# Optimization experiments

Hardware: AMD Instinct MI355X
Metric: run time of the kernel (lower is better)

## Reference

```python
import jax, jax.numpy as jnp
import numpy as np

DK = 64

def setup_inputs() -> dict:
    key = jax.random.key(0)
    kx, kq, kk, kv = jax.random.split(key, 4)
    B, T, DM, DV = 256, 256, 384, 64
    x = jax.random.normal(kx, (B, T, DM), dtype=jnp.float32)
    s = 1.0 / np.sqrt(DM)
    W_q = jax.random.normal(kq, (DM, DK), dtype=jnp.float32) * s
    W_k = jax.random.normal(kk, (DM, DK), dtype=jnp.float32) * s
    W_v = jax.random.normal(kv, (DM, DV), dtype=jnp.float32) * s
    return {"x": x, "W_q": W_q, "W_k": W_k, "W_v": W_v}

def reference(x, W_q, W_k, W_v):
    # x: [B, T, dm]; projections to [B, T, dk]/[B, T, dv]
    q = jnp.einsum('btc,ck->btk', x, W_q)
    k = jnp.einsum('btc,ck->btk', x, W_k)
    v = jnp.einsum('btc,cv->btv', x, W_v)
    scale = k.shape[-1] ** (-0.5)
    wei = jnp.einsum('btk,bsk->bts', q, k) * scale  # [B, T, T]
    T = x.shape[1]
    causal = jnp.tril(jnp.ones((T, T), dtype=bool))
    wei = jnp.where(causal, wei, -jnp.inf)
    wei = jax.nn.softmax(wei, axis=-1)
    # dropout omitted (eval mode / deterministic reference)
    out = jnp.einsum('bts,bsv->btv', wei, v)
    return out
```

## Files before the change

### kernel.cpp

```cpp
#include <hip/hip_runtime.h>


typedef __attribute__((ext_vector_type(8))) short short8;
typedef __attribute__((ext_vector_type(4))) float floatx4;

__device__ inline unsigned short f2bf(float f) {
  union { float f; unsigned u; } v; v.f = f;
  unsigned r = v.u + 0x7FFFu + ((v.u >> 16) & 1u);
  return (unsigned short)(r >> 16);
}

__global__ void wt_kernel(const float* __restrict__ wq, const float* __restrict__ wk,
                          const float* __restrict__ wv, unsigned short* __restrict__ wt) {
  int idx = blockIdx.x * 256 + threadIdx.x;
  if (idx >= 3 * 384 * 64) return;
  int mat = idx / (384 * 64);
  int rem = idx % (384 * 64);
  int k = rem >> 6, n = rem & 63;
  const float* w = (mat == 0) ? wq : ((mat == 1) ? wk : wv);
  wt[((size_t)mat * 64 + n) * 384 + k] = f2bf(w[rem]);
}

__global__ __launch_bounds__(256) void qkv_kernel(
    const float* __restrict__ x, const unsigned short* __restrict__ wt,
    unsigned short* __restrict__ q, unsigned short* __restrict__ k2,
    unsigned short* __restrict__ v) {
  int lane = threadIdx.x & 63;
  int wave = threadIdx.x >> 6;
  int m = lane & 15, quad = lane >> 4;
  int tokBase = blockIdx.x * 128 + wave * 32;

  floatx4 z = {0.f, 0.f, 0.f, 0.f};
  floatx4 acc[2][12];
#pragma unroll
  for (int a = 0; a < 2; ++a)
#pragma unroll
    for (int b = 0; b < 12; ++b) acc[a][b] = z;

#pragma unroll
  for (int ks = 0; ks < 12; ++ks) {
    short8 af[2];
#pragma unroll
    for (int mt = 0; mt < 2; ++mt) {
      const float* ap = x + (size_t)(tokBase + mt * 16 + m) * 384 + ks * 32 + quad * 8;
      float4 x0 = *(const float4*)ap;
      float4 x1 = *(const float4*)(ap + 4);
      short8 t;
      t[0] = (short)f2bf(x0.x); t[1] = (short)f2bf(x0.y);
      t[2] = (short)f2bf(x0.z); t[3] = (short)f2bf(x0.w);
      t[4] = (short)f2bf(x1.x); t[5] = (short)f2bf(x1.y);
      t[6] = (short)f2bf(x1.z); t[7] = (short)f2bf(x1.w);
      af[mt] = t;
    }
#pragma unroll
    for (int nt = 0; nt < 12; ++nt) {
      const short8 bf = *(const short8*)&wt[((size_t)(nt >> 2) * 64 + (nt & 3) * 16 + m) * 384 + ks * 32 + quad * 8];
      acc[0][nt] = __builtin_amdgcn_mfma_f32_16x16x32_bf16(af[0], bf, acc[0][nt], 0, 0, 0);
      acc[1][nt] = __builtin_amdgcn_mfma_f32_16x16x32_bf16(af[1], bf, acc[1][nt], 0, 0, 0);
    }
  }

#pragma unroll
  for (int mt = 0; mt < 2; ++mt)
#pragma unroll
    for (int nt = 0; nt < 12; ++nt) {
      unsigned short* op = (nt < 4) ? q : ((nt < 8) ? k2 : v);
      int ncol = (nt & 3) * 16;
#pragma unroll
      for (int j = 0; j < 4; ++j) {
        int row = tokBase + mt * 16 + quad * 4 + j;
        op[(size_t)row * 64 + ncol + m] = f2bf(acc[mt][nt][j]);
      }
    }
}

__global__ __launch_bounds__(256) void attn_kernel(
    const unsigned short* __restrict__ Q, const unsigned short* __restrict__ K,
    const unsigned short* __restrict__ V, float* __restrict__ out) {
  __shared__ __align__(16) unsigned short sK[256 * 72];
  __shared__ __align__(16) unsigned short sV[64 * 264];

  int tid = threadIdx.x;
  int lane = tid & 63, wave = tid >> 6;
  int m = lane & 15, quad = lane >> 4;
  int b = blockIdx.x >> 2, qt = blockIdx.x & 3;

  const unsigned short* Kg = K + (size_t)b * 256 * 64;
#pragma unroll
  for (int it = 0; it < 8; ++it) {
    int s = it * 32 + (tid >> 3);
    int c = (tid & 7) * 8;
    *(uint4*)&sK[s * 72 + c] = *(const uint4*)&Kg[s * 64 + c];
  }
  const unsigned short* Vg = V + (size_t)b * 256 * 64;
#pragma unroll 4
  for (int it = 0; it < 64; ++it) {
    int idx = it * 256 + tid;
    sV[(idx & 63) * 264 + (idx >> 6)] = Vg[idx];
  }

  int qrow = qt * 64 + wave * 16 + m;
  const unsigned short* Qg = Q + ((size_t)b * 256 + qrow) * 64;
  short8 qf0 = *(const short8*)&Qg[quad * 8];
  short8 qf1 = *(const short8*)&Qg[32 + quad * 8];

  __syncthreads();

  floatx4 z = {0.f, 0.f, 0.f, 0.f};
  floatx4 sacc[16];
#pragma unroll
  for (int nt = 0; nt < 16; ++nt) sacc[nt] = z;
#pragma unroll
  for (int nt = 0; nt < 16; ++nt) {
    short8 kb0 = *(const short8*)&sK[(nt * 16 + m) * 72 + quad * 8];
    short8 kb1 = *(const short8*)&sK[(nt * 16 + m) * 72 + 32 + quad * 8];
    sacc[nt] = __builtin_amdgcn_mfma_f32_16x16x32_bf16(qf0, kb0, sacc[nt], 0, 0, 0);
    sacc[nt] = __builtin_amdgcn_mfma_f32_16x16x32_bf16(qf1, kb1, sacc[nt], 0, 0, 0);
  }

  const float CSC = 0.18033688011112042f;
  const float NEG = -3.0e38f;
  float inv[4];
  int rbase = qt * 64 + wave * 16 + quad * 4;
#pragma unroll
  for (int j = 0; j < 4; ++j) {
    int rg = rbase + j;
    float mx = NEG;
#pragma unroll
    for (int nt = 0; nt < 16; ++nt) {
      int col = nt * 16 + m;
      float sv = sacc[nt][j];
      if (col > rg) { sv = NEG; sacc[nt][j] = sv; }
      mx = fmaxf(mx, sv);
    }
    mx = fmaxf(mx, __shfl_xor(mx, 1));
    mx = fmaxf(mx, __shfl_xor(mx, 2));
    mx = fmaxf(mx, __shfl_xor(mx, 4));
    mx = fmaxf(mx, __shfl_xor(mx, 8));
    float sum = 0.f;
#pragma unroll
    for (int nt = 0; nt < 16; ++nt) {
      float p = exp2f((sacc[nt][j] - mx) * CSC);
      sacc[nt][j] = p;
      sum += p;
    }
    sum += __shfl_xor(sum, 1);
    sum += __shfl_xor(sum, 2);
    sum += __shfl_xor(sum, 4);
    sum += __shfl_xor(sum, 8);
    inv[j] = 1.f / sum;
  }

  __syncthreads();

  unsigned short* sP = sK + wave * (16 * 264);
#pragma unroll
  for (int nt = 0; nt < 16; ++nt)
#pragma unroll
    for (int j = 0; j < 4; ++j)
      sP[(quad * 4 + j) * 264 + nt * 16 + m] = f2bf(sacc[nt][j] * inv[j]);

  __syncthreads();

  floatx4 o[4];
#pragma unroll
  for (int vt = 0; vt < 4; ++vt) o[vt] = z;
#pragma unroll
  for (int ks = 0; ks < 8; ++ks) {
    short8 pf = *(const short8*)&sP[m * 264 + ks * 32 + quad * 8];
#pragma unroll
    for (int vt = 0; vt < 4; ++vt) {
      short8 vb = *(const short8*)&sV[(vt * 16 + m) * 264 + ks * 32 + quad * 8];
      o[vt] = __builtin_amdgcn_mfma_f32_16x16x32_bf16(pf, vb, o[vt], 0, 0, 0);
    }
  }

  float* op = out + ((size_t)b * 256 + qt * 64 + wave * 16) * 64;
#pragma unroll
  for (int vt = 0; vt < 4; ++vt)
#pragma unroll
    for (int j = 0; j < 4; ++j)
      op[(quad * 4 + j) * 64 + vt * 16 + m] = o[vt][j];
}

extern "C" void kernel_launch(void* const* d_in, const int* in_sizes, int n_in,
                              void* d_out, int out_size, void* d_ws, size_t ws_size,
                              hipStream_t stream) {
  const float* x  = (const float*)d_in[0];
  const float* wq = (const float*)d_in[1];
  const float* wk = (const float*)d_in[2];
  const float* wv = (const float*)d_in[3];
  float* out = (float*)d_out;

  unsigned short* wt = (unsigned short*)d_ws;
  unsigned short* q  = (unsigned short*)((char*)d_ws + 147456);
  unsigned short* k  = q + (size_t)65536 * 64;
  unsigned short* v  = k + (size_t)65536 * 64;

  wt_kernel<<<288, 256, 0, stream>>>(wq, wk, wv, wt);
  qkv_kernel<<<512, 256, 0, stream>>>(x, wt, q, k, v);
  attn_kernel<<<256 * 4, 256, 0, stream>>>(q, k, v, out);
}
```

Measured before the change: 209.9 us.

## Stage QKV projection tiles via async LDS loads and emit transposed V

The QKV projection kernel now double-buffers x and weight tiles in LDS using global_load_lds with XOR swizzles. Each block handles 64 tokens, and each wave owns 48 output columns instead of reading operands straight from global memory per wave. V is written transposed through an LDS tile, so the attention kernel can load it with 16-byte vector copies instead of scalar transposing stores. The weight-transpose kernel is also remapped so its writes are coalesced. Together these aim to cut redundant global traffic and the slow scalar V transpose, at the cost of more LDS use and extra barriers.

Measured after the change: 194.5 us. 7.3% less time.

```diff
diff --git a/kernel.cpp b/kernel.cpp
--- a/kernel.cpp
+++ b/kernel.cpp
@@ -10,73 +10,129 @@
   return (unsigned short)(r >> 16);
 }
 
+__device__ inline void glds16(const void* g, void* l) {
+  __builtin_amdgcn_global_load_lds(
+      (const __attribute__((address_space(1))) void*)g,
+      (__attribute__((address_space(3))) void*)l, 16, 0, 0);
+}
+
 __global__ void wt_kernel(const float* __restrict__ wq, const float* __restrict__ wk,
                           const float* __restrict__ wv, unsigned short* __restrict__ wt) {
   int idx = blockIdx.x * 256 + threadIdx.x;
-  if (idx >= 3 * 384 * 64) return;
-  int mat = idx / (384 * 64);
-  int rem = idx % (384 * 64);
-  int k = rem >> 6, n = rem & 63;
+  if (idx >= 3 * 64 * 384) return;
+  int mat = idx / (64 * 384);
+  int rem = idx % (64 * 384);
+  int n = rem / 384, k = rem % 384;
   const float* w = (mat == 0) ? wq : ((mat == 1) ? wk : wv);
-  wt[((size_t)mat * 64 + n) * 384 + k] = f2bf(w[rem]);
-}
-
-__global__ __launch_bounds__(256) void qkv_kernel(
+  wt[idx] = f2bf(w[k * 64 + n]);
+}
+
+__global__ __launch_bounds__(256, 4) void qkv_kernel(
     const float* __restrict__ x, const unsigned short* __restrict__ wt,
-    unsigned short* __restrict__ q, unsigned short* __restrict__ k2,
-    unsigned short* __restrict__ v) {
-  int lane = threadIdx.x & 63;
-  int wave = threadIdx.x >> 6;
+    unsigned short* __restrict__ q, unsigned short* __restrict__ kk,
+    unsigned short* __restrict__ vt) {
+  __shared__ __align__(16) float          xa[2][64 * 32];
+  __shared__ __align__(16) unsigned short wb[2][192 * 32];
+
+  int tid = threadIdx.x, lane = tid & 63, w = tid >> 6;
   int m = lane & 15, quad = lane >> 4;
-  int tokBase = blockIdx.x * 128 + wave * 32;
+  int tok0 = blockIdx.x * 64;
 
   floatx4 z = {0.f, 0.f, 0.f, 0.f};
-  floatx4 acc[2][12];
-#pragma unroll
-  for (int a = 0; a < 2; ++a)
-#pragma unroll
-    for (int b = 0; b < 12; ++b) acc[a][b] = z;
-
-#pragma unroll
+  floatx4 acc[4][3];
+#pragma unroll
+  for (int a = 0; a < 4; ++a)
+#pragma unroll
+    for (int b = 0; b < 3; ++b) acc[a][b] = z;
+
+  auto stage = [&](int ks, int buf) {
+#pragma unroll
+    for (int i = 0; i < 2; ++i) {
+      int a = w * 2 + i;
+      int row = a * 8 + (lane >> 3);
+      int kq = (lane & 7) ^ (row & 7);
+      glds16(x + (size_t)(tok0 + row) * 384 + ks * 32 + kq * 4,
+             (void*)&xa[buf][a * 256]);
+    }
+#pragma unroll
+    for (int i = 0; i < 3; ++i) {
+      int g = w * 3 + i;
+      int c = g * 16 + (lane >> 2);
+      int kq = (lane & 3) ^ (c & 3) ^ ((c >> 2) & 3);
+      glds16(wt + (size_t)c * 384 + ks * 32 + kq * 8,
+             (void*)&wb[buf][g * 512]);
+    }
+  };
+
+  stage(0, 0);
+#pragma unroll 1
   for (int ks = 0; ks < 12; ++ks) {
-    short8 af[2];
-#pragma unroll
-    for (int mt = 0; mt < 2; ++mt) {
-      const float* ap = x + (size_t)(tokBase + mt * 16 + m) * 384 + ks * 32 + quad * 8;
-      float4 x0 = *(const float4*)ap;
-      float4 x1 = *(const float4*)(ap + 4);
+    int buf = ks & 1;
+    __syncthreads();
+    if (ks < 11) stage(ks + 1, buf ^ 1);
+
+    short8 af[4];
+#pragma unroll
+    for (int mt = 0; mt < 4; ++mt) {
+      int r = mt * 16 + m;
+      int s0 = (2 * quad) ^ (m & 7);
+      int s1 = (2 * quad + 1) ^ (m & 7);
+      float4 f0 = *(const float4*)&xa[buf][r * 32 + s0 * 4];
+      float4 f1 = *(const float4*)&xa[buf][r * 32 + s1 * 4];
       short8 t;
-      t[0] = (short)f2bf(x0.x); t[1] = (short)f2bf(x0.y);
-      t[2] = (short)f2bf(x0.z); t[3] = (short)f2bf(x0.w);
-      t[4] = (short)f2bf(x1.x); t[5] = (short)f2bf(x1.y);
-      t[6] = (short)f2bf(x1.z); t[7] = (short)f2bf(x1.w);
+      t[0] = (short)f2bf(f0.x); t[1] = (short)f2bf(f0.y);
+      t[2] = (short)f2bf(f0.z); t[3] = (short)f2bf(f0.w);
+      t[4] = (short)f2bf(f1.x); t[5] = (short)f2bf(f1.y);
+      t[6] = (short)f2bf(f1.z); t[7] = (short)f2bf(f1.w);
       af[mt] = t;
     }
-#pragma unroll
-    for (int nt = 0; nt < 12; ++nt) {
-      const short8 bf = *(const short8*)&wt[((size_t)(nt >> 2) * 64 + (nt & 3) * 16 + m) * 384 + ks * 32 + quad * 8];
-      acc[0][nt] = __builtin_amdgcn_mfma_f32_16x16x32_bf16(af[0], bf, acc[0][nt], 0, 0, 0);
-      acc[1][nt] = __builtin_amdgcn_mfma_f32_16x16x32_bf16(af[1], bf, acc[1][nt], 0, 0, 0);
-    }
-  }
-
-#pragma unroll
-  for (int mt = 0; mt < 2; ++mt)
-#pragma unroll
-    for (int nt = 0; nt < 12; ++nt) {
-      unsigned short* op = (nt < 4) ? q : ((nt < 8) ? k2 : v);
-      int ncol = (nt & 3) * 16;
+    short8 bf[3];
+#pragma unroll
+    for (int nt = 0; nt < 3; ++nt) {
+      int c = w * 48 + nt * 16 + m;
+      int sq = quad ^ (c & 3) ^ ((c >> 2) & 3);
+      bf[nt] = *(const short8*)&wb[buf][c * 32 + sq * 8];
+    }
+#pragma unroll
+    for (int mt = 0; mt < 4; ++mt)
+#pragma unroll
+      for (int nt = 0; nt < 3; ++nt)
+        acc[mt][nt] = __builtin_amdgcn_mfma_f32_16x16x32_bf16(af[mt], bf[nt], acc[mt][nt], 0, 0, 0);
+  }
+
+  __syncthreads();
+  unsigned short* vtile = (unsigned short*)&xa[0][0];
+
+#pragma unroll
+  for (int mt = 0; mt < 4; ++mt)
+#pragma unroll
+    for (int nt = 0; nt < 3; ++nt) {
+      int cb = w * 48 + nt * 16;
 #pragma unroll
       for (int j = 0; j < 4; ++j) {
-        int row = tokBase + mt * 16 + quad * 4 + j;
-        op[(size_t)row * 64 + ncol + m] = f2bf(acc[mt][nt][j]);
+        int row = mt * 16 + quad * 4 + j;
+        unsigned short val = f2bf(acc[mt][nt][j]);
+        if (cb < 64)        q [(size_t)(tok0 + row) * 64 + cb + m]       = val;
+        else if (cb < 128)  kk[(size_t)(tok0 + row) * 64 + cb - 64 + m]  = val;
+        else                vtile[(cb - 128 + m) * 72 + row] = val;
       }
     }
+
+  __syncthreads();
+  {
+    int c = tid >> 2, t4 = tid & 3;
+    int bb = tok0 >> 8, tm = tok0 & 255;
+    uint4 d0 = *(const uint4*)&vtile[c * 72 + t4 * 16];
+    uint4 d1 = *(const uint4*)&vtile[c * 72 + t4 * 16 + 8];
+    size_t base = ((size_t)bb * 64 + c) * 256 + tm + t4 * 16;
+    *(uint4*)&vt[base]     = d0;
+    *(uint4*)&vt[base + 8] = d1;
+  }
 }
 
 __global__ __launch_bounds__(256) void attn_kernel(
     const unsigned short* __restrict__ Q, const unsigned short* __restrict__ K,
-    const unsigned short* __restrict__ V, float* __restrict__ out) {
+    const unsigned short* __restrict__ Vt, float* __restrict__ out) {
   __shared__ __align__(16) unsigned short sK[256 * 72];
   __shared__ __align__(16) unsigned short sV[64 * 264];
 
@@ -92,11 +148,11 @@
     int c = (tid & 7) * 8;
     *(uint4*)&sK[s * 72 + c] = *(const uint4*)&Kg[s * 64 + c];
   }
-  const unsigned short* Vg = V + (size_t)b * 256 * 64;
-#pragma unroll 4
-  for (int it = 0; it < 64; ++it) {
-    int idx = it * 256 + tid;
-    sV[(idx & 63) * 264 + (idx >> 6)] = Vg[idx];
+  const unsigned short* Vg = Vt + (size_t)b * 64 * 256;
+#pragma unroll
+  for (int it = 0; it < 8; ++it) {
+    int lin = it * 2048 + tid * 8;
+    *(uint4*)&sV[(lin >> 8) * 264 + (lin & 255)] = *(const uint4*)&Vg[lin];
   }
 
   int qrow = qt * 64 + wave * 16 + m;
@@ -195,9 +251,9 @@
   unsigned short* wt = (unsigned short*)d_ws;
   unsigned short* q  = (unsigned short*)((char*)d_ws + 147456);
   unsigned short* k  = q + (size_t)65536 * 64;
-  unsigned short* v  = k + (size_t)65536 * 64;
+  unsigned short* vt = k + (size_t)65536 * 64;
 
   wt_kernel<<<288, 256, 0, stream>>>(wq, wk, wv, wt);
-  qkv_kernel<<<512, 256, 0, stream>>>(x, wt, q, k, v);
-  attn_kernel<<<256 * 4, 256, 0, stream>>>(q, k, v, out);
-}
+  qkv_kernel<<<1024, 256, 0, stream>>>(x, wt, q, k, vt);
+  attn_kernel<<<256 * 4, 256, 0, stream>>>(q, k, vt, out);
+}
```

## Fuse QKV projection and causal attention into one per-batch kernel

Applied to the files above, without the earlier changes.

Merges the QKV projection and attention kernels into a single 1024-thread block per batch. Q, K and V^T are written straight to LDS instead of round-tripping through global memory, and x/W tiles are staged with swizzled global_load_lds. Causal structure is exploited by skipping key tiles beyond each wave's diagonal in both QK^T and PV. The cost is fewer, larger blocks (256) with heavy LDS use and a serialized 12-step projection loop with barriers, which may limit occupancy and latency hiding.

Result: faster. 178.1 us (-15.1%).

```diff
diff --git a/kernel.cpp b/kernel.cpp
--- a/kernel.cpp
+++ b/kernel.cpp
@@ -10,124 +10,117 @@
   return (unsigned short)(r >> 16);
 }
 
+__device__ inline void glds16(const void* g, void* l) {
+  __builtin_amdgcn_global_load_lds(
+      (const __attribute__((address_space(1))) void*)g,
+      (__attribute__((address_space(3))) void*)l, 16, 0, 0);
+}
+
 __global__ void wt_kernel(const float* __restrict__ wq, const float* __restrict__ wk,
                           const float* __restrict__ wv, unsigned short* __restrict__ wt) {
   int idx = blockIdx.x * 256 + threadIdx.x;
-  if (idx >= 3 * 384 * 64) return;
-  int mat = idx / (384 * 64);
-  int rem = idx % (384 * 64);
-  int k = rem >> 6, n = rem & 63;
+  if (idx >= 3 * 64 * 384) return;
+  int mat = idx / (64 * 384);
+  int rem = idx % (64 * 384);
+  int n = rem / 384, k = rem % 384;
   const float* w = (mat == 0) ? wq : ((mat == 1) ? wk : wv);
-  wt[((size_t)mat * 64 + n) * 384 + k] = f2bf(w[rem]);
+  wt[idx] = f2bf(w[k * 64 + n]);
 }
 
-__global__ __launch_bounds__(256) void qkv_kernel(
+__global__ __launch_bounds__(1024, 4) void fused_kernel(
     const float* __restrict__ x, const unsigned short* __restrict__ wt,
-    unsigned short* __restrict__ q, unsigned short* __restrict__ k2,
-    unsigned short* __restrict__ v) {
-  int lane = threadIdx.x & 63;
-  int wave = threadIdx.x >> 6;
-  int m = lane & 15, quad = lane >> 4;
-  int tokBase = blockIdx.x * 128 + wave * 32;
+    float* __restrict__ out) {
+  __shared__ __align__(16) unsigned short sK[256 * 72];
+  __shared__ __align__(16) unsigned short sVT[64 * 264];
+  __shared__ __align__(16) unsigned char stg[45056];
+  float* xa = (float*)stg;
+  unsigned short* wb = (unsigned short*)(stg + 32768);
+
+  int tid = threadIdx.x, lane = tid & 63, w = tid >> 6;
+  int m = lane & 15, q = lane >> 4;
+  int b = blockIdx.x;
+  const float* xb = x + (size_t)b * 256 * 384;
 
   floatx4 z = {0.f, 0.f, 0.f, 0.f};
-  floatx4 acc[2][12];
+  floatx4 acc[12];
 #pragma unroll
-  for (int a = 0; a < 2; ++a)
+  for (int nt = 0; nt < 12; ++nt) acc[nt] = z;
+
+#pragma unroll 1
+  for (int ks = 0; ks < 12; ++ks) {
 #pragma unroll
-    for (int b = 0; b < 12; ++b) acc[a][b] = z;
+    for (int i = 0; i < 2; ++i) {
+      int a = 2 * w + i;
+      int row = a * 8 + (lane >> 3);
+      int g = (lane & 7) ^ (row & 7);
+      glds16(xb + (size_t)row * 384 + ks * 32 + g * 4, (void*)(xa + a * 256));
+    }
+    if (w < 12) {
+      int c = w * 16 + (lane >> 2);
+      int g = (lane & 3) ^ (c & 3);
+      glds16(wt + (size_t)c * 384 + ks * 32 + g * 8, (void*)(wb + w * 512));
+    }
+    __syncthreads();
+
+    int r = w * 16 + m;
+    int s0 = (2 * q) ^ (m & 7);
+    float4 f0 = *(const float4*)(xa + r * 32 + s0 * 4);
+    float4 f1 = *(const float4*)(xa + r * 32 + (s0 ^ 1) * 4);
+    short8 af;
+    af[0] = (short)f2bf(f0.x); af[1] = (short)f2bf(f0.y);
+    af[2] = (short)f2bf(f0.z); af[3] = (short)f2bf(f0.w);
+    af[4] = (short)f2bf(f1.x); af[5] = (short)f2bf(f1.y);
+    af[6] = (short)f2bf(f1.z); af[7] = (short)f2bf(f1.w);
 
 #pragma unroll
-  for (int ks = 0; ks < 12; ++ks) {
-    short8 af[2];
+    for (int nt = 0; nt < 12; ++nt) {
+      int sq = q ^ (m & 3);
+      short8 bf = *(const short8*)(wb + (nt * 16 + m) * 32 + sq * 8);
+      acc[nt] = __builtin_amdgcn_mfma_f32_16x16x32_bf16(af, bf, acc[nt], 0, 0, 0);
+    }
+    __syncthreads();
+  }
+
+  unsigned short* scr = (unsigned short*)stg + w * 1152;
 #pragma unroll
-    for (int mt = 0; mt < 2; ++mt) {
-      const float* ap = x + (size_t)(tokBase + mt * 16 + m) * 384 + ks * 32 + quad * 8;
-      float4 x0 = *(const float4*)ap;
-      float4 x1 = *(const float4*)(ap + 4);
-      short8 t;
-      t[0] = (short)f2bf(x0.x); t[1] = (short)f2bf(x0.y);
-      t[2] = (short)f2bf(x0.z); t[3] = (short)f2bf(x0.w);
-      t[4] = (short)f2bf(x1.x); t[5] = (short)f2bf(x1.y);
-      t[6] = (short)f2bf(x1.z); t[7] = (short)f2bf(x1.w);
-      af[mt] = t;
-    }
+  for (int nt = 0; nt < 12; ++nt) {
 #pragma unroll
-    for (int nt = 0; nt < 12; ++nt) {
-      const short8 bf = *(const short8*)&wt[((size_t)(nt >> 2) * 64 + (nt & 3) * 16 + m) * 384 + ks * 32 + quad * 8];
-      acc[0][nt] = __builtin_amdgcn_mfma_f32_16x16x32_bf16(af[0], bf, acc[0][nt], 0, 0, 0);
-      acc[1][nt] = __builtin_amdgcn_mfma_f32_16x16x32_bf16(af[1], bf, acc[1][nt], 0, 0, 0);
+    for (int j = 0; j < 4; ++j) {
+      unsigned short val = f2bf(acc[nt][j]);
+      int lrow = q * 4 + j;
+      int grow = w * 16 + lrow;
+      if (nt < 4)       scr[lrow * 72 + nt * 16 + m] = val;
+      else if (nt < 8)  sK[grow * 72 + (nt - 4) * 16 + m] = val;
+      else              sVT[((nt - 8) * 16 + m) * 264 + grow] = val;
     }
   }
 
-#pragma unroll
-  for (int mt = 0; mt < 2; ++mt)
-#pragma unroll
-    for (int nt = 0; nt < 12; ++nt) {
-      unsigned short* op = (nt < 4) ? q : ((nt < 8) ? k2 : v);
-      int ncol = (nt & 3) * 16;
-#pragma unroll
-      for (int j = 0; j < 4; ++j) {
-        int row = tokBase + mt * 16 + quad * 4 + j;
-        op[(size_t)row * 64 + ncol + m] = f2bf(acc[mt][nt][j]);
-      }
-    }
-}
-
-__global__ __launch_bounds__(256) void attn_kernel(
-    const unsigned short* __restrict__ Q, const unsigned short* __restrict__ K,
-    const unsigned short* __restrict__ V, float* __restrict__ out) {
-  __shared__ __align__(16) unsigned short sK[256 * 72];
-  __shared__ __align__(16) unsigned short sV[64 * 264];
-
-  int tid = threadIdx.x;
-  int lane = tid & 63, wave = tid >> 6;
-  int m = lane & 15, quad = lane >> 4;
-  int b = blockIdx.x >> 2, qt = blockIdx.x & 3;
-
-  const unsigned short* Kg = K + (size_t)b * 256 * 64;
-#pragma unroll
-  for (int it = 0; it < 8; ++it) {
-    int s = it * 32 + (tid >> 3);
-    int c = (tid & 7) * 8;
-    *(uint4*)&sK[s * 72 + c] = *(const uint4*)&Kg[s * 64 + c];
-  }
-  const unsigned short* Vg = V + (size_t)b * 256 * 64;
-#pragma unroll 4
-  for (int it = 0; it < 64; ++it) {
-    int idx = it * 256 + tid;
-    sV[(idx & 63) * 264 + (idx >> 6)] = Vg[idx];
-  }
-
-  int qrow = qt * 64 + wave * 16 + m;
-  const unsigned short* Qg = Q + ((size_t)b * 256 + qrow) * 64;
-  short8 qf0 = *(const short8*)&Qg[quad * 8];
-  short8 qf1 = *(const short8*)&Qg[32 + quad * 8];
+  short8 qf0 = *(const short8*)(scr + m * 72 + q * 8);
+  short8 qf1 = *(const short8*)(scr + m * 72 + 32 + q * 8);
 
   __syncthreads();
 
-  floatx4 z = {0.f, 0.f, 0.f, 0.f};
   floatx4 sacc[16];
 #pragma unroll
-  for (int nt = 0; nt < 16; ++nt) sacc[nt] = z;
-#pragma unroll
   for (int nt = 0; nt < 16; ++nt) {
-    short8 kb0 = *(const short8*)&sK[(nt * 16 + m) * 72 + quad * 8];
-    short8 kb1 = *(const short8*)&sK[(nt * 16 + m) * 72 + 32 + quad * 8];
-    sacc[nt] = __builtin_amdgcn_mfma_f32_16x16x32_bf16(qf0, kb0, sacc[nt], 0, 0, 0);
-    sacc[nt] = __builtin_amdgcn_mfma_f32_16x16x32_bf16(qf1, kb1, sacc[nt], 0, 0, 0);
+    if (nt > w) continue;
+    short8 kb0 = *(const short8*)(sK + (nt * 16 + m) * 72 + q * 8);
+    short8 kb1 = *(const short8*)(sK + (nt * 16 + m) * 72 + 32 + q * 8);
+    floatx4 t = __builtin_amdgcn_mfma_f32_16x16x32_bf16(qf0, kb0, z, 0, 0, 0);
+    sacc[nt] = __builtin_amdgcn_mfma_f32_16x16x32_bf16(qf1, kb1, t, 0, 0, 0);
   }
 
   const float CSC = 0.18033688011112042f;
   const float NEG = -3.0e38f;
-  float inv[4];
-  int rbase = qt * 64 + wave * 16 + quad * 4;
+  float inv_[4];
+  int rbase = w * 16 + q * 4;
 #pragma unroll
   for (int j = 0; j < 4; ++j) {
     int rg = rbase + j;
     float mx = NEG;
 #pragma unroll
     for (int nt = 0; nt < 16; ++nt) {
+      if (nt > w) continue;
       int col = nt * 16 + m;
       float sv = sacc[nt][j];
       if (col > rg) { sv = NEG; sacc[nt][j] = sv; }
@@ -140,6 +133,7 @@
     float sum = 0.f;
 #pragma unroll
     for (int nt = 0; nt < 16; ++nt) {
+      if (nt > w) continue;
       float p = exp2f((sacc[nt][j] - mx) * CSC);
       sacc[nt][j] = p;
       sum += p;
@@ -148,39 +142,41 @@
     sum += __shfl_xor(sum, 2);
     sum += __shfl_xor(sum, 4);
     sum += __shfl_xor(sum, 8);
-    inv[j] = 1.f / sum;
+    inv_[j] = 1.f / sum;
   }
-
-  __syncthreads();
-
-  unsigned short* sP = sK + wave * (16 * 264);
-#pragma unroll
-  for (int nt = 0; nt < 16; ++nt)
-#pragma unroll
-    for (int j = 0; j < 4; ++j)
-      sP[(quad * 4 + j) * 264 + nt * 16 + m] = f2bf(sacc[nt][j] * inv[j]);
-
-  __syncthreads();
 
   floatx4 o[4];
 #pragma unroll
   for (int vt = 0; vt < 4; ++vt) o[vt] = z;
 #pragma unroll
-  for (int ks = 0; ks < 8; ++ks) {
-    short8 pf = *(const short8*)&sP[m * 264 + ks * 32 + quad * 8];
+  for (int c = 0; c < 4; ++c) {
+    if (4 * c > w) continue;
+#pragma unroll
+    for (int t = 0; t < 4; ++t) {
+      int nt = 4 * c + t;
+#pragma unroll
+      for (int j = 0; j < 4; ++j) {
+        unsigned short pv = (nt <= w) ? f2bf(sacc[nt][j] * inv_[j]) : (unsigned short)0;
+        scr[(q * 4 + j) * 72 + t * 16 + m] = pv;
+      }
+    }
+    short8 pf0 = *(const short8*)(scr + m * 72 + q * 8);
+    short8 pf1 = *(const short8*)(scr + m * 72 + 32 + q * 8);
 #pragma unroll
     for (int vt = 0; vt < 4; ++vt) {
-      short8 vb = *(const short8*)&sV[(vt * 16 + m) * 264 + ks * 32 + quad * 8];
-      o[vt] = __builtin_amdgcn_mfma_f32_16x16x32_bf16(pf, vb, o[vt], 0, 0, 0);
+      short8 vb0 = *(const short8*)(sVT + (vt * 16 + m) * 264 + c * 64 + q * 8);
+      short8 vb1 = *(const short8*)(sVT + (vt * 16 + m) * 264 + c * 64 + 32 + q * 8);
+      o[vt] = __builtin_amdgcn_mfma_f32_16x16x32_bf16(pf0, vb0, o[vt], 0, 0, 0);
+      o[vt] = __builtin_amdgcn_mfma_f32_16x16x32_bf16(pf1, vb1, o[vt], 0, 0, 0);
     }
   }
 
-  float* op = out + ((size_t)b * 256 + qt * 64 + wave * 16) * 64;
+  float* op = out + ((size_t)b * 256 + w * 16) * 64;
 #pragma unroll
   for (int vt = 0; vt < 4; ++vt)
 #pragma unroll
     for (int j = 0; j < 4; ++j)
-      op[(quad * 4 + j) * 64 + vt * 16 + m] = o[vt][j];
+      op[(q * 4 + j) * 64 + vt * 16 + m] = o[vt][j];
 }
 
 extern "C" void kernel_launch(void* const* d_in, const int* in_sizes, int n_in,
@@ -193,11 +189,7 @@
   float* out = (float*)d_out;
 
   unsigned short* wt = (unsigned short*)d_ws;
-  unsigned short* q  = (unsigned short*)((char*)d_ws + 147456);
-  unsigned short* k  = q + (size_t)65536 * 64;
-  unsigned short* v  = k + (size_t)65536 * 64;
 
   wt_kernel<<<288, 256, 0, stream>>>(wq, wk, wv, wt);
-  qkv_kernel<<<512, 256, 0, stream>>>(x, wt, q, k, v);
-  attn_kernel<<<256 * 4, 256, 0, stream>>>(q, k, v, out);
+  fused_kernel<<<256, 1024, 0, stream>>>(x, wt, out);
 }
```
